# Optimization experiments

Measured on AMD Instinct MI355X. Metric: run time of the kernel, lower is better.

Reference implementation:

```python
import jax, jax.numpy as jnp
import numpy as np

EPS = 1e-4


def setup_inputs() -> dict:
    key = jax.random.key(0)
    k1, k2, k3, k4, k5 = jax.random.split(key, 5)
    N, M, F = 2048, 2048, 128
    embeds = jax.random.uniform(k1, (N, F), dtype=jnp.float32)
    base_embeds = jax.random.normal(k2, (M, F), dtype=jnp.float32)
    base_rewards = jax.random.normal(k3, (M,), dtype=jnp.float32)
    # torch Linear(num_feat, num_feat, bias=False) / Linear(num_feat, 1, bias=False)
    # stored here as [in, out] for x @ W convention
    W1 = jax.random.normal(k4, (F, F), dtype=jnp.float32) / np.sqrt(F)
    w2 = jax.random.normal(k5, (F, 1), dtype=jnp.float32) / np.sqrt(F)
    return {"embeds": embeds, "base_embeds": base_embeds,
            "base_rewards": base_rewards, "W1": W1, "w2": w2}


def reference(embeds, base_embeds, base_rewards, W1, w2):
    # pairwise differences: [N, M, F]
    diff = embeds[:, None, :] - base_embeds[None, :, :]
    # tiny MLP distance kernel: Linear -> ELU -> Linear, abs
    h = jax.nn.elu(jnp.einsum('nmf,fg->nmg', diff, W1))
    dist = jnp.abs(jnp.einsum('nmg,go->nmo', h, w2)[:, :, 0])  # [N, M]
    # inverse-distance normalized weights
    dist_w = 1.0 / (dist + EPS)
    dist_w = dist_w / jnp.sum(dist_w, axis=1, keepdims=True)
    rewards = jnp.sum(dist_w * base_rewards[None, :], axis=1)  # [N]
    return rewards
```

## Files before the change

### kernel.cpp

```cpp
#include <hip/hip_runtime.h>
#include <hip/hip_bf16.h>

#define F      128
#define NROWS  2048
#define MROWS  2048
#define BN     64
#define BM     64
#define MT     (MROWS/BM)
#define GC     16
#define NCH    (F/GC)
#define LW     20
#define LOG2E  1.44269504088896340736f

typedef float f32x4 __attribute__((ext_vector_type(4)));

__global__ __launch_bounds__(256) void proj_kernel(
    const float* __restrict__ embeds, const float* __restrict__ base,
    const float* __restrict__ W1, const float* __restrict__ w2,
    float* __restrict__ A1W, float* __restrict__ AEW,
    float* __restrict__ B1W, float* __restrict__ BEp,
    float* __restrict__ w2sum)
{
    const int tid = threadIdx.x;
    const int sub = tid >> 7;
    const int g   = tid & 127;
    const int row = blockIdx.x * 2 + sub;

    __shared__ float xs[2][F];
    {
        const float* src = (row < NROWS) ? &embeds[(size_t)row * F]
                                         : &base[(size_t)(row - NROWS) * F];
        xs[sub][g] = src[g];
    }
    __syncthreads();

    float acc = 0.0f;
#pragma unroll 8
    for (int f = 0; f < F; ++f)
        acc = fmaf(xs[sub][f], W1[f * F + g], acc);

    const float w = w2[g];
    if (row < NROWS) {
        const size_t idx = (size_t)row * F + g;
        A1W[idx] = (acc + 1.0f) * w;
        AEW[idx] = __builtin_amdgcn_exp2f(acc * LOG2E) * w;
    } else {
        const size_t idx = (size_t)(row - NROWS) * F + g;
        B1W[idx] = acc * w;
        BEp[idx] = __builtin_amdgcn_exp2f(-acc * LOG2E);
    }

    if (blockIdx.x == 0 && tid < 64) {
        float s = w2[tid] + w2[tid + 64];
#pragma unroll
        for (int k = 1; k < 64; k <<= 1) s += __shfl_xor(s, k);
        if (tid == 0) *w2sum = s;
    }
}

__global__ __launch_bounds__(64) void pair_kernel(
    const float* __restrict__ A1W, const float* __restrict__ AEW,
    const float* __restrict__ B1W, const float* __restrict__ BEp,
    const float* __restrict__ w2, const float* __restrict__ w2sum_p,
    const float* __restrict__ brew, float* __restrict__ partials)
{
    __shared__ float sA1[BN][LW], sAE[BN][LW];
    __shared__ float sB1[BM][LW], sBE[BM][LW];

    const int lane = threadIdx.x;
    const int nt   = blockIdx.x;
    const int mt   = blockIdx.y;
    const int n0   = nt * BN;
    const int m0   = mt * BM;
    const int tr   = lane >> 3;
    const int tc   = lane & 7;

    const float* pA1 = A1W + (size_t)n0 * F;
    const float* pAE = AEW + (size_t)n0 * F;
    const float* pB1 = B1W + (size_t)m0 * F;
    const float* pBE = BEp + (size_t)m0 * F;

    float acc[8][8];
#pragma unroll
    for (int i = 0; i < 8; ++i)
#pragma unroll
        for (int j = 0; j < 8; ++j) acc[i][j] = 0.0f;

#define STAGE_PLANE(SRC, DST)                                              \
    _Pragma("unroll")                                                      \
    for (int rnd = 0; rnd < 4; ++rnd) {                                    \
        const int idx = rnd * 64 + lane;                                   \
        const int r = idx >> 2, c = (idx & 3) * 4;                         \
        *(f32x4*)&DST[r][c] = *(const f32x4*)&SRC[(size_t)r * F + g0 + c]; \
    }

#pragma unroll 1
    for (int ch = 0; ch < NCH; ++ch) {
        const int g0 = ch * GC;
        STAGE_PLANE(pA1, sA1)
        STAGE_PLANE(pAE, sAE)
        STAGE_PLANE(pB1, sB1)
        STAGE_PLANE(pBE, sBE)

#pragma unroll 1
        for (int g4 = 0; g4 < GC; g4 += 4) {
            const f32x4 wv = *(const f32x4*)&w2[g0 + g4];
            f32x4 b1v[8], bev[8];
#pragma unroll
            for (int j = 0; j < 8; ++j) {
                b1v[j] = *(const f32x4*)&sB1[tc + 8 * j][g4];
                bev[j] = *(const f32x4*)&sBE[tc + 8 * j][g4];
            }
#pragma unroll
            for (int i = 0; i < 8; ++i) {
                const f32x4 a1 = *(const f32x4*)&sA1[tr + 8 * i][g4];
                const f32x4 ae = *(const f32x4*)&sAE[tr + 8 * i][g4];
#pragma unroll
                for (int j = 0; j < 8; ++j) {
                    float d = acc[i][j];
                    d += __builtin_amdgcn_fmed3f(a1.x - b1v[j].x, ae.x * bev[j].x, wv.x);
                    d += __builtin_amdgcn_fmed3f(a1.y - b1v[j].y, ae.y * bev[j].y, wv.y);
                    d += __builtin_amdgcn_fmed3f(a1.z - b1v[j].z, ae.z * bev[j].z, wv.z);
                    d += __builtin_amdgcn_fmed3f(a1.w - b1v[j].w, ae.w * bev[j].w, wv.w);
                    acc[i][j] = d;
                }
            }
        }
    }
#undef STAGE_PLANE

    const float w2sum = *w2sum_p;
    float rsv[8];
#pragma unroll
    for (int j = 0; j < 8; ++j) rsv[j] = brew[m0 + tc + 8 * j];

#pragma unroll
    for (int i = 0; i < 8; ++i) {
        float sw = 0.0f, swr = 0.0f;
#pragma unroll
        for (int j = 0; j < 8; ++j) {
            const float dist = fabsf(acc[i][j] - w2sum);
            const float w = 1.0f / (dist + 1e-4f);
            sw += w;
            swr = fmaf(w, rsv[j], swr);
        }
#pragma unroll
        for (int k = 1; k < 8; k <<= 1) {
            sw  += __shfl_xor(sw, k);
            swr += __shfl_xor(swr, k);
        }
        if (tc == 0) {
            const int n = n0 + tr + 8 * i;
            partials[((size_t)n * MT + mt) * 2 + 0] = sw;
            partials[((size_t)n * MT + mt) * 2 + 1] = swr;
        }
    }
}

__global__ __launch_bounds__(256) void finalize_kernel(
    const float* __restrict__ partials, float* __restrict__ out)
{
    const int n = blockIdx.x * 256 + threadIdx.x;
    if (n < NROWS) {
        float sw = 0.0f, swr = 0.0f;
#pragma unroll
        for (int t = 0; t < MT; ++t) {
            sw  += partials[((size_t)n * MT + t) * 2 + 0];
            swr += partials[((size_t)n * MT + t) * 2 + 1];
        }
        out[n] = swr / sw;
    }
}

extern "C" void kernel_launch(void* const* d_in, const int* in_sizes, int n_in,
                              void* d_out, int out_size, void* d_ws, size_t ws_size,
                              hipStream_t stream)
{
    const float* embeds       = (const float*)d_in[0];
    const float* base_embeds  = (const float*)d_in[1];
    const float* base_rewards = (const float*)d_in[2];
    const float* W1           = (const float*)d_in[3];
    const float* w2           = (const float*)d_in[4];
    float* out = (float*)d_out;

    float* partials = (float*)d_ws;
    float* A1W = partials + (size_t)NROWS * MT * 2;
    float* AEW = A1W + (size_t)NROWS * F;
    float* B1W = AEW + (size_t)NROWS * F;
    float* BEp = B1W + (size_t)MROWS * F;
    float* w2s = BEp + (size_t)MROWS * F;

    proj_kernel<<<(NROWS + MROWS) / 2, 256, 0, stream>>>(
        embeds, base_embeds, W1, w2, A1W, AEW, B1W, BEp, w2s);

    dim3 grid2(NROWS / BN, MROWS / BM);
    pair_kernel<<<grid2, 64, 0, stream>>>(A1W, AEW, B1W, BEp, w2, w2s, base_rewards, partials);

    finalize_kernel<<<(NROWS + 255) / 256, 256, 0, stream>>>(partials, out);
}
```

Before: 89.15 us.

## Enlarge pair tiles, double-buffer LDS staging, and use packed f32 ops

The pair kernel now uses 128x128 tiles with 256 threads, and the planes are interleaved into combined LDS arrays. The next chunk is prefetched into registers and written to a second LDS buffer, so global loads overlap with compute. The inner loop uses v_pk_add/v_pk_mul packed FP32 ops, with B1W pre-negated in the projection so a packed add replaces the subtract. The aim is to cut VALU instruction count and staging stalls, at the cost of more register pressure and fewer blocks per device (256 vs 1024), which may lower occupancy.

After: 261.6 us. 2.93x slower.

```diff
diff --git a/kernel.cpp b/kernel.cpp
--- a/kernel.cpp
+++ b/kernel.cpp
@@ -4,15 +4,25 @@
 #define F      128
 #define NROWS  2048
 #define MROWS  2048
-#define BN     64
-#define BM     64
+#define BN     128
+#define BM     128
 #define MT     (MROWS/BM)
 #define GC     16
 #define NCH    (F/GC)
-#define LW     20
+#define LW     36
 #define LOG2E  1.44269504088896340736f
 
+typedef float f32x2 __attribute__((ext_vector_type(2)));
 typedef float f32x4 __attribute__((ext_vector_type(4)));
+
+__device__ __forceinline__ f32x2 lo2(f32x4 v) { return __builtin_shufflevector(v, v, 0, 1); }
+__device__ __forceinline__ f32x2 hi2(f32x4 v) { return __builtin_shufflevector(v, v, 2, 3); }
+__device__ __forceinline__ f32x2 pk_add(f32x2 a, f32x2 b) {
+    f32x2 d; asm("v_pk_add_f32 %0, %1, %2" : "=v"(d) : "v"(a), "v"(b)); return d;
+}
+__device__ __forceinline__ f32x2 pk_mul(f32x2 a, f32x2 b) {
+    f32x2 d; asm("v_pk_mul_f32 %0, %1, %2" : "=v"(d) : "v"(a), "v"(b)); return d;
+}
 
 __global__ __launch_bounds__(256) void proj_kernel(
     const float* __restrict__ embeds, const float* __restrict__ base,
@@ -46,7 +56,7 @@
         AEW[idx] = __builtin_amdgcn_exp2f(acc * LOG2E) * w;
     } else {
         const size_t idx = (size_t)(row - NROWS) * F + g;
-        B1W[idx] = acc * w;
+        B1W[idx] = -acc * w;
         BEp[idx] = __builtin_amdgcn_exp2f(-acc * LOG2E);
     }
 
@@ -58,27 +68,22 @@
     }
 }
 
-__global__ __launch_bounds__(64) void pair_kernel(
+__global__ __launch_bounds__(256) void pair_kernel(
     const float* __restrict__ A1W, const float* __restrict__ AEW,
     const float* __restrict__ B1W, const float* __restrict__ BEp,
     const float* __restrict__ w2, const float* __restrict__ w2sum_p,
     const float* __restrict__ brew, float* __restrict__ partials)
 {
-    __shared__ float sA1[BN][LW], sAE[BN][LW];
-    __shared__ float sB1[BM][LW], sBE[BM][LW];
-
-    const int lane = threadIdx.x;
-    const int nt   = blockIdx.x;
-    const int mt   = blockIdx.y;
-    const int n0   = nt * BN;
-    const int m0   = mt * BM;
-    const int tr   = lane >> 3;
-    const int tc   = lane & 7;
-
-    const float* pA1 = A1W + (size_t)n0 * F;
-    const float* pAE = AEW + (size_t)n0 * F;
-    const float* pB1 = B1W + (size_t)m0 * F;
-    const float* pBE = BEp + (size_t)m0 * F;
+    __shared__ float sA[2][BN][LW];
+    __shared__ float sB[2][BM][LW];
+
+    const int tid = threadIdx.x;
+    const int nt  = blockIdx.x;
+    const int mt  = blockIdx.y;
+    const int n0  = nt * BN;
+    const int m0  = mt * BM;
+    const int tr  = tid >> 4;
+    const int tc  = tid & 15;
 
     float acc[8][8];
 #pragma unroll
@@ -86,53 +91,82 @@
 #pragma unroll
         for (int j = 0; j < 8; ++j) acc[i][j] = 0.0f;
 
-#define STAGE_PLANE(SRC, DST)                                              \
-    _Pragma("unroll")                                                      \
-    for (int rnd = 0; rnd < 4; ++rnd) {                                    \
-        const int idx = rnd * 64 + lane;                                   \
-        const int r = idx >> 2, c = (idx & 3) * 4;                         \
-        *(f32x4*)&DST[r][c] = *(const f32x4*)&SRC[(size_t)r * F + g0 + c]; \
-    }
+    f32x4 rA[4], rB[4];
+
+#define LOADCH(G0)                                                             \
+    { _Pragma("unroll")                                                        \
+      for (int rnd = 0; rnd < 4; ++rnd) {                                      \
+          const int idx = rnd * 256 + tid;                                     \
+          const int r = idx >> 3, c4 = idx & 7;                                \
+          const float* sa = (c4 < 4) ? A1W : AEW;                              \
+          const float* sb = (c4 < 4) ? B1W : BEp;                              \
+          const int col = (G0) + (c4 & 3) * 4;                                 \
+          rA[rnd] = *(const f32x4*)&sa[(size_t)(n0 + r) * F + col];            \
+          rB[rnd] = *(const f32x4*)&sb[(size_t)(m0 + r) * F + col];            \
+      } }
+
+#define WRITECH(BUF)                                                           \
+    { _Pragma("unroll")                                                        \
+      for (int rnd = 0; rnd < 4; ++rnd) {                                      \
+          const int idx = rnd * 256 + tid;                                     \
+          const int r = idx >> 3, c4 = idx & 7;                                \
+          *(f32x4*)&sA[BUF][r][c4 * 4] = rA[rnd];                              \
+          *(f32x4*)&sB[BUF][r][c4 * 4] = rB[rnd];                              \
+      } }
+
+    LOADCH(0)
+    WRITECH(0)
+    __syncthreads();
 
 #pragma unroll 1
     for (int ch = 0; ch < NCH; ++ch) {
-        const int g0 = ch * GC;
-        STAGE_PLANE(pA1, sA1)
-        STAGE_PLANE(pAE, sAE)
-        STAGE_PLANE(pB1, sB1)
-        STAGE_PLANE(pBE, sBE)
-
-#pragma unroll 1
+        const int g0  = ch * GC;
+        const int buf = ch & 1;
+
+        if (ch + 1 < NCH) LOADCH(g0 + GC)
+
+#pragma unroll
         for (int g4 = 0; g4 < GC; g4 += 4) {
-            const f32x4 wv = *(const f32x4*)&w2[g0 + g4];
+            const f32x4 wq = *(const f32x4*)&w2[g0 + g4];
             f32x4 b1v[8], bev[8];
 #pragma unroll
             for (int j = 0; j < 8; ++j) {
-                b1v[j] = *(const f32x4*)&sB1[tc + 8 * j][g4];
-                bev[j] = *(const f32x4*)&sBE[tc + 8 * j][g4];
+                b1v[j] = *(const f32x4*)&sB[buf][tc + 16 * j][g4];
+                bev[j] = *(const f32x4*)&sB[buf][tc + 16 * j][16 + g4];
             }
 #pragma unroll
             for (int i = 0; i < 8; ++i) {
-                const f32x4 a1 = *(const f32x4*)&sA1[tr + 8 * i][g4];
-                const f32x4 ae = *(const f32x4*)&sAE[tr + 8 * i][g4];
+                const f32x4 a1 = *(const f32x4*)&sA[buf][tr + 16 * i][g4];
+                const f32x4 ae = *(const f32x4*)&sA[buf][tr + 16 * i][16 + g4];
+                const f32x2 a1l = lo2(a1), a1h = hi2(a1);
+                const f32x2 ael = lo2(ae), aeh = hi2(ae);
 #pragma unroll
                 for (int j = 0; j < 8; ++j) {
-                    float d = acc[i][j];
-                    d += __builtin_amdgcn_fmed3f(a1.x - b1v[j].x, ae.x * bev[j].x, wv.x);
-                    d += __builtin_amdgcn_fmed3f(a1.y - b1v[j].y, ae.y * bev[j].y, wv.y);
-                    d += __builtin_amdgcn_fmed3f(a1.z - b1v[j].z, ae.z * bev[j].z, wv.z);
-                    d += __builtin_amdgcn_fmed3f(a1.w - b1v[j].w, ae.w * bev[j].w, wv.w);
-                    acc[i][j] = d;
+                    const f32x2 x1l = pk_add(a1l, lo2(b1v[j]));
+                    const f32x2 eel = pk_mul(ael, lo2(bev[j]));
+                    const f32x2 x1h = pk_add(a1h, hi2(b1v[j]));
+                    const f32x2 eeh = pk_mul(aeh, hi2(bev[j]));
+                    f32x2 s1, s2;
+                    s1.x = __builtin_amdgcn_fmed3f(x1l.x, eel.x, wq.x);
+                    s1.y = __builtin_amdgcn_fmed3f(x1l.y, eel.y, wq.y);
+                    s2.x = __builtin_amdgcn_fmed3f(x1h.x, eeh.x, wq.z);
+                    s2.y = __builtin_amdgcn_fmed3f(x1h.y, eeh.y, wq.w);
+                    const f32x2 t = pk_add(s1, s2);
+                    acc[i][j] += t.x + t.y;
                 }
             }
         }
-    }
-#undef STAGE_PLANE
+
+        if (ch + 1 < NCH) WRITECH((ch + 1) & 1)
+        __syncthreads();
+    }
+#undef LOADCH
+#undef WRITECH
 
     const float w2sum = *w2sum_p;
     float rsv[8];
 #pragma unroll
-    for (int j = 0; j < 8; ++j) rsv[j] = brew[m0 + tc + 8 * j];
+    for (int j = 0; j < 8; ++j) rsv[j] = brew[m0 + tc + 16 * j];
 
 #pragma unroll
     for (int i = 0; i < 8; ++i) {
@@ -145,12 +179,12 @@
             swr = fmaf(w, rsv[j], swr);
         }
 #pragma unroll
-        for (int k = 1; k < 8; k <<= 1) {
+        for (int k = 1; k < 16; k <<= 1) {
             sw  += __shfl_xor(sw, k);
             swr += __shfl_xor(swr, k);
         }
         if (tc == 0) {
-            const int n = n0 + tr + 8 * i;
+            const int n = n0 + tr + 16 * i;
             partials[((size_t)n * MT + mt) * 2 + 0] = sw;
             partials[((size_t)n * MT + mt) * 2 + 1] = swr;
         }
@@ -194,7 +228,7 @@
         embeds, base_embeds, W1, w2, A1W, AEW, B1W, BEp, w2s);
 
     dim3 grid2(NROWS / BN, MROWS / BM);
-    pair_kernel<<<grid2, 64, 0, stream>>>(A1W, AEW, B1W, BEp, w2, w2s, base_rewards, partials);
+    pair_kernel<<<grid2, 256, 0, stream>>>(A1W, AEW, B1W, BEp, w2, w2s, base_rewards, partials);
 
     finalize_kernel<<<(NROWS + 255) / 256, 256, 0, stream>>>(partials, out);
 }
```
